# Kernel optimization log

Measured on AMD Instinct MI355X. Metric: run time of the kernel, lower is better.

Reference implementation:

```python
import jax, jax.numpy as jnp
import numpy as np

B, CIN, COUT, G, HEADS = 4, 256, 256, 8, 4
K, S, P = 7, 1, 3
H = W = 32
IN_W = CIN // G
OUT_W = COUT // G


def setup_inputs() -> dict:
    key = jax.random.key(0)
    ks = jax.random.split(key, 9)
    def n(k, shape, scale=1.0):
        return jax.random.normal(k, shape, dtype=jnp.float32) * scale
    # kaiming fan_out init for the 1x1 convs (fan_out = out channels)
    return {
        "x": n(ks[0], (B, CIN, H, W)),
        "wq": n(ks[1], (G, OUT_W * HEADS, IN_W), (2.0 / (OUT_W * HEADS)) ** 0.5),
        "bq": n(ks[2], (G, OUT_W * HEADS), 0.01),
        "wk": n(ks[3], (G, OUT_W, IN_W), (2.0 / OUT_W) ** 0.5),
        "bk": n(ks[4], (G, OUT_W), 0.01),
        "wv": n(ks[5], (G, OUT_W, IN_W), (2.0 / OUT_W) ** 0.5),
        "bv": n(ks[6], (G, OUT_W), 0.01),
        "rel_h": n(ks[7], (OUT_W // 2, 1, 1, G, K, 1)),
        "rel_w": n(ks[8], (OUT_W // 2, 1, 1, G, 1, K)),
    }


def _sparse_conv(x, w, b):
    # grouped 1x1 conv, groups stacked on last axis (matches torch.stack(dim=-1))
    # x: [B, G*I, h, w]; w: [G, O, I]; b: [G, O] -> [B, O, h, w, G]
    Bn, C, hh, ww = x.shape
    xr = x.reshape(Bn, G, C // G, hh, ww)
    out = jnp.einsum('bgihw,goi->bohwg', xr, w)
    return out + b.T[None, :, None, None, :]


def _unfold(x5, k, s):
    # x5: [B, C, Hp, Wp, G] -> [B, C, Ho, Wo, G, k, k]  (torch unfold(2).unfold(3))
    Bn, C, Hp, Wp, Gn = x5.shape
    Ho = (Hp - k) // s + 1
    Wo = (Wp - k) // s + 1
    patches = jnp.stack(
        [x5[:, :, i:i + (Ho - 1) * s + 1:s, j:j + (Wo - 1) * s + 1:s, :]
         for i in range(k) for j in range(k)], axis=-1)
    return patches.reshape(Bn, C, Ho, Wo, Gn, k, k)


def reference(x, wq, bq, wk, bk, wv, bv, rel_h, rel_w):
    xp = jnp.pad(x, ((0, 0), (0, 0), (P, P), (P, P)))
    q = _sparse_conv(x, wq, bq)    # [B, OUT_W*HEADS, H, W, G]
    k = _sparse_conv(xp, wk, bk)   # [B, OUT_W, Hp, Wp, G] (bias at padded locations, as in torch)
    v = _sparse_conv(xp, wv, bv)
    k = _unfold(k, K, S)           # [B, OUT_W, H, W, G, K, K]
    v = _unfold(v, K, S)
    kh, kw = jnp.split(k, 2, axis=1)
    k = jnp.concatenate([kh + rel_h, kw + rel_w], axis=1)
    kf = k.reshape(B, OUT_W, H, W, G * K * K)
    vf = v.reshape(B, OUT_W, H, W, G * K * K)
    q = q.reshape(B, HEADS, OUT_W, H, W, G)
    # scores: sum over channel c; softmax over flattened (group, kh, kw) window
    scores = jnp.einsum('bhcxyg,bcxym->bhxygm', q, kf)
    attn = jax.nn.softmax(scores, axis=-1)
    # weighted sum over window m and heads h (matches sum(dim=1) then sum(dim=-1))
    out = jnp.einsum('bhxygm,bcxym->bcxyg', attn, vf)   # [B, OUT_W, H, W, G]
    out = jnp.transpose(out, (0, 4, 2, 3, 1)).reshape(B, -1, H, W)  # transpose(1,-1)+reshape
    return out
```

## Files before the change

### kernel.cpp

```cpp
#include <hip/hip_runtime.h>
#include <math.h>

typedef _Float16 f16;
typedef _Float16 f16x4 __attribute__((ext_vector_type(4)));
typedef _Float16 f16x8 __attribute__((ext_vector_type(8)));
typedef __bf16 bf16x4 __attribute__((ext_vector_type(4)));
typedef __bf16 bf16x4a8 __attribute__((ext_vector_type(4), aligned(8)));
typedef short s16x4 __attribute__((ext_vector_type(4)));
typedef float f32x4 __attribute__((ext_vector_type(4)));

#define MFMA_F16(a, b, c)  __builtin_amdgcn_mfma_f32_16x16x32_f16(a, b, c, 0, 0, 0)
#define MFMA_BF16_K16(a, b, c) __builtin_amdgcn_mfma_f32_16x16x16bf16_1k(a, b, c, 0, 0, 0)

#define VSS 12160

static __device__ inline f16x8 cvt8(const float* p) {
    const float4* p4 = (const float4*)p;
    float4 u0 = p4[0], u1 = p4[1];
    f16x8 r;
    r[0] = (f16)u0.x; r[1] = (f16)u0.y; r[2] = (f16)u0.z; r[3] = (f16)u0.w;
    r[4] = (f16)u1.x; r[5] = (f16)u1.y; r[6] = (f16)u1.z; r[7] = (f16)u1.w;
    return r;
}

__global__ __launch_bounds__(256) void produce_kernel(
    const float* __restrict__ x,
    const float* __restrict__ wq, const float* __restrict__ bq,
    const float* __restrict__ wk, const float* __restrict__ bk,
    const float* __restrict__ wv, const float* __restrict__ bv,
    const float* __restrict__ rel_h, const float* __restrict__ rel_w,
    f16* __restrict__ Qb, f16* __restrict__ Kb,
    __bf16* __restrict__ V4, f16* __restrict__ relp) {
    int bid = blockIdx.x;
    int t = threadIdx.x;

    if (bid == 1216) {
        for (int idx = t; idx < 448 * 32; idx += 256) {
            int c = idx & 31, key = idx >> 5;
            int kw = key & 7, ghk = key >> 3;
            int gp = (ghk * 37) >> 8;
            int kh = ghk - gp * 7;
            float v = 0.f;
            if (kw < 7)
                v = (c < 16) ? rel_h[c * 56 + gp * 7 + kh]
                             : rel_w[(c - 16) * 56 + gp * 7 + kw];
            relp[idx] = (f16)v;
        }
        return;
    }

    int hp = bid % 38, g = (bid / 38) & 7, b = bid / 304;
    bool hin = (hp >= 3 && hp < 35);
    size_t kvbase = (size_t)(b * 8 + g);
    size_t rowp = (kvbase * 38 + hp) * 10;

    if (!hin) {
        for (int idx = t; idx < 38 * 32; idx += 256) {
            int wp = idx >> 5, c = idx & 31;
            Kb[((kvbase * 38 + hp) * 38 + wp) * 32 + c] = (f16)bk[g * 32 + c];
        }
        for (int idx = t; idx < 4 * 40 * 32; idx += 256) {
            int c = idx & 31, w = (idx >> 5) % 40, s = (idx >> 5) / 40;
            int wp = s + w;
            __bf16 val = (wp <= 37) ? (__bf16)bv[g * 32 + c] : (__bf16)0.f;
            V4[((size_t)s * VSS + rowp + (w >> 2)) * 128 + c * 4 + (w & 3)] = val;
        }
        return;
    }

    int h = hp - 3;
    __shared__ __align__(16) f16 xTl[32 * 40];
    __shared__ float vt[32 * 44];

    {
        int ic = t >> 3, w = (t & 7) * 4;
        float4 xv = *(const float4*)(x + (((size_t)b * 256 + g * 32 + ic) * 32 + h) * 32 + w);
        xTl[(w + 0) * 40 + ic] = (f16)xv.x;
        xTl[(w + 1) * 40 + ic] = (f16)xv.y;
        xTl[(w + 2) * 40 + ic] = (f16)xv.z;
        xTl[(w + 3) * 40 + ic] = (f16)xv.w;
    }
    for (int idx = t; idx < 384; idx += 256) {
        int c = idx & 31, wi = idx >> 5;
        float bb = bv[g * 32 + c];
        if (wi < 3) vt[c * 44 + wi] = bb;
        else if (wi < 6) vt[c * 44 + 32 + wi] = bb;
        else vt[c * 44 + 32 + wi] = 0.f;
    }
    __syncthreads();

    int l15 = t & 15, quad = (t >> 4) & 3, wave = t >> 6;

    f16x8 xf0 = *(const f16x8*)(xTl + l15 * 40 + quad * 8);
    f16x8 xf1 = *(const f16x8*)(xTl + (16 + l15) * 40 + quad * 8);

#pragma unroll
    for (int i = 0; i < 2; ++i) {
        int mq = wave * 2 + i;
        f16x8 wf = cvt8(wq + ((size_t)g * 128 + mq * 16 + l15) * 32 + quad * 8);
        float4 b4 = *(const float4*)(bq + g * 128 + mq * 16 + quad * 4);
#pragma unroll
        for (int Nt = 0; Nt < 2; ++Nt) {
            f32x4 d = {0.f, 0.f, 0.f, 0.f};
            d = MFMA_F16(wf, Nt ? xf1 : xf0, d);
            f16x4 q4;
            q4[0] = (f16)(d[0] + b4.x); q4[1] = (f16)(d[1] + b4.y);
            q4[2] = (f16)(d[2] + b4.z); q4[3] = (f16)(d[3] + b4.w);
            int w = Nt * 16 + l15;
            *(f16x4*)(Qb + (size_t)((b * 32 + h) * 32 + w) * 1024 + g * 128 + mq * 16 + quad * 4) = q4;
        }
    }

    if (wave < 2) {
        f16x8 wf = cvt8(wk + ((size_t)g * 32 + wave * 16 + l15) * 32 + quad * 8);
        float4 b4 = *(const float4*)(bk + g * 32 + wave * 16 + quad * 4);
#pragma unroll
        for (int Nt = 0; Nt < 2; ++Nt) {
            f32x4 d = {0.f, 0.f, 0.f, 0.f};
            d = MFMA_F16(wf, Nt ? xf1 : xf0, d);
            f16x4 k4;
            k4[0] = (f16)(d[0] + b4.x); k4[1] = (f16)(d[1] + b4.y);
            k4[2] = (f16)(d[2] + b4.z); k4[3] = (f16)(d[3] + b4.w);
            int wp = Nt * 16 + l15 + 3;
            *(f16x4*)(Kb + ((kvbase * 38 + hp) * 38 + wp) * 32 + wave * 16 + quad * 4) = k4;
        }
    } else {
        int Nt = wave - 2;
        f16x8 wf = cvt8(wv + ((size_t)g * 32 + Nt * 16 + l15) * 32 + quad * 8);
        float bias = bv[g * 32 + Nt * 16 + l15];
        int c = Nt * 16 + l15;
#pragma unroll
        for (int Mt = 0; Mt < 2; ++Mt) {
            f32x4 d = {0.f, 0.f, 0.f, 0.f};
            d = MFMA_F16(Mt ? xf1 : xf0, wf, d);
            int wp0 = Mt * 16 + quad * 4 + 3;
            vt[c * 44 + wp0 + 0] = d[0] + bias;
            vt[c * 44 + wp0 + 1] = d[1] + bias;
            vt[c * 44 + wp0 + 2] = d[2] + bias;
            vt[c * 44 + wp0 + 3] = d[3] + bias;
        }
    }

    for (int idx = t; idx < 192; idx += 256) {
        int wi = idx >> 5, c = idx & 31;
        int wp = (wi < 3) ? wi : (32 + wi);
        Kb[((kvbase * 38 + hp) * 38 + wp) * 32 + c] = (f16)bk[g * 32 + c];
    }
    __syncthreads();

    for (int idx = t; idx < 1280; idx += 256) {
        int c = idx & 31;
        int p = (idx >> 5) % 10;
        int s = (idx >> 5) / 10;
        const float* src = vt + c * 44 + s + p * 4;
        bf16x4a8 q;
        q[0] = (__bf16)src[0]; q[1] = (__bf16)src[1];
        q[2] = (__bf16)src[2]; q[3] = (__bf16)src[3];
        *(bf16x4a8*)(V4 + ((size_t)s * VSS + rowp + p) * 128 + c * 4) = q;
    }
}

__global__ __launch_bounds__(256, 4) void attn_kernel(
    const f16* __restrict__ Qb, const f16* __restrict__ Kb,
    const __bf16* __restrict__ V4, const f16* __restrict__ relp,
    float* __restrict__ out) {
    int bid = blockIdx.x;
    int t = threadIdx.x;
    int wvi = t >> 6;
    int pid = (bid & 7) * 512 + (bid >> 3);
    int y = pid & 31, x = (pid >> 5) & 31, b = pid >> 10;

    __shared__ __align__(16) float accS[3 * 64 * 20];

    int lane = t & 63;
    int l15 = lane & 15, quad = lane >> 4, kwl = lane & 7, p8 = (lane >> 3) & 1;
    bool oddq = (quad & 1);

    f16x8 qf[2];
    {
        const f16* qp = Qb + (size_t)pid * 1024;
        qf[0] = *(const f16x8*)(qp + l15 * 32 + quad * 8);
        qf[1] = *(const f16x8*)(qp + (16 + l15) * 32 + quad * 8);
    }

    float fsumT[2] = {0.f, 0.f};
    f32x4 acc[2][2];
#pragma unroll
    for (int ct = 0; ct < 2; ++ct)
#pragma unroll
        for (int m = 0; m < 2; ++m) acc[ct][m] = (f32x4){0.f, 0.f, 0.f, 0.f};

    int yk = y + kwl;
    if (yk > 37) yk = 37;
    size_t vshift = (size_t)(y & 3) * VSS;

    {
        int chunk = wvi;
        int gpr = chunk * 2 + p8;
        int gpv = chunk * 2 + (quad >> 1);
        const f16* kbp = Kb + ((((size_t)(b * 8 + gpr) * 38 + x) * 38 + yk) << 5) + quad * 8;
        const f16* rpp = relp + ((size_t)(gpr * 56 + kwl) << 5) + quad * 8;
        const __bf16* vp0 = V4 +
            ((vshift + ((size_t)(b * 8 + gpv) * 38 + x) * 10 + (y >> 2) + (quad & 1)) << 7) +
            l15 * 4;
        const __bf16* vp1 = vp0 + 64;
#pragma unroll
        for (int kh = 0; kh < 7; ++kh) {
            f16x8 kb = *(const f16x8*)kbp;  kbp += 38 * 32;
            f16x8 rp = *(const f16x8*)rpp;  rpp += 256;
            s16x4 vf0 = *(const s16x4*)vp0;  vp0 += 1280;
            s16x4 vf1 = *(const s16x4*)vp1;  vp1 += 1280;
            kb += rp;
#pragma unroll
            for (int Mt = 0; Mt < 2; ++Mt) {
                f32x4 d = {0.f, 0.f, 0.f, 0.f};
                d = MFMA_F16(kb, qf[Mt], d);
                float e0 = __expf(d[0]);
                float e1 = __expf(d[1]);
                float e2 = __expf(d[2]);
                float e3 = oddq ? 0.f : __expf(d[3]);
                fsumT[Mt] += (e0 + e1) + (e2 + e3);
                bf16x4 pb;
                pb[0] = (__bf16)e0; pb[1] = (__bf16)e1;
                pb[2] = (__bf16)e2; pb[3] = (__bf16)e3;
                s16x4 pbi = __builtin_bit_cast(s16x4, pb);
                acc[0][Mt] = MFMA_BF16_K16(vf0, pbi, acc[0][Mt]);
                acc[1][Mt] = MFMA_BF16_K16(vf1, pbi, acc[1][Mt]);
            }
        }
    }

#pragma unroll
    for (int m = 0; m < 2; ++m) {
        fsumT[m] += __shfl_xor(fsumT[m], 16);
        fsumT[m] += __shfl_xor(fsumT[m], 32);
    }

    if (wvi != 0) {
        float* sp = accS + ((wvi - 1) * 64 + lane) * 20;
        *(f32x4*)(sp + 0)  = acc[0][0];
        *(f32x4*)(sp + 4)  = acc[0][1];
        *(f32x4*)(sp + 8)  = acc[1][0];
        *(f32x4*)(sp + 12) = acc[1][1];
        sp[16] = fsumT[0];
        sp[17] = fsumT[1];
    }
    __syncthreads();
    if (wvi != 0) return;

#pragma unroll
    for (int wsrc = 0; wsrc < 3; ++wsrc) {
        const float* sp = accS + (wsrc * 64 + lane) * 20;
        acc[0][0] += *(const f32x4*)(sp + 0);
        acc[0][1] += *(const f32x4*)(sp + 4);
        acc[1][0] += *(const f32x4*)(sp + 8);
        acc[1][1] += *(const f32x4*)(sp + 12);
        fsumT[0] += sp[16];
        fsumT[1] += sp[17];
    }
    float inv[2] = {1.0f / fsumT[0], 1.0f / fsumT[1]};

#pragma unroll
    for (int Mt = 0; Mt < 2; ++Mt)
#pragma unroll
        for (int ct = 0; ct < 2; ++ct) {
            float v[4];
#pragma unroll
            for (int r = 0; r < 4; ++r) {
                v[r] = acc[ct][Mt][r] * inv[Mt];
                v[r] += __shfl_xor(v[r], 1);
                v[r] += __shfl_xor(v[r], 2);
            }
            if ((l15 & 3) == 0) {
                int g = Mt * 4 + (l15 >> 2);
                float4 o4 = {v[0], v[1], v[2], v[3]};
                *(float4*)(out + ((((size_t)(b * 8 + g) * 32 + x) * 32 + y) << 5) +
                           ct * 16 + quad * 4) = o4;
            }
        }
}

extern "C" void kernel_launch(void* const* d_in, const int* in_sizes, int n_in,
                              void* d_out, int out_size, void* d_ws, size_t ws_size,
                              hipStream_t stream) {
    const float* x     = (const float*)d_in[0];
    const float* wq    = (const float*)d_in[1];
    const float* bq    = (const float*)d_in[2];
    const float* wk    = (const float*)d_in[3];
    const float* bk    = (const float*)d_in[4];
    const float* wv    = (const float*)d_in[5];
    const float* bv    = (const float*)d_in[6];
    const float* rel_h = (const float*)d_in[7];
    const float* rel_w = (const float*)d_in[8];
    float* out = (float*)d_out;

    unsigned char* ws = (unsigned char*)d_ws;
    f16*    Qb   = (f16*)ws;
    f16*    Kb   = (f16*)(ws + 8388608);
    __bf16* V4   = (__bf16*)(ws + 8388608 + 2957312);
    f16*    relp = (f16*)(ws + 8388608 + 2957312 + 12451840);

    hipLaunchKernelGGL(produce_kernel, dim3(1217), dim3(256), 0, stream,
                       x, wq, bq, wk, bk, wv, bv, rel_h, rel_w, Qb, Kb, V4, relp);
    hipLaunchKernelGGL(attn_kernel, dim3(4096), dim3(256), 0, stream,
                       Qb, Kb, V4, relp, out);
}
```

Baseline: 120.4 us.

## Tile attention over 8 output columns with shared K/V windows in LDS

The attention kernel now handles 8 adjacent y positions per 512-thread block, with one wave per position instead of four waves per position. The overlapping K and V windows are staged once into LDS and reused across those positions. V is stored in a compact single-copy layout rather than four shifted copies, and the unaligned bf16 pairs are recovered with funnel-shift selects. The cross-wave LDS reduction is removed. In exchange, LDS use is large and occupancy falls to one block per CU.

Measured after the change: 121.6 us. About the same (+1.0%).

```diff
diff --git a/kernel.cpp b/kernel.cpp
--- a/kernel.cpp
+++ b/kernel.cpp
@@ -8,11 +8,10 @@
 typedef __bf16 bf16x4a8 __attribute__((ext_vector_type(4), aligned(8)));
 typedef short s16x4 __attribute__((ext_vector_type(4)));
 typedef float f32x4 __attribute__((ext_vector_type(4)));
+typedef unsigned int u32;
 
 #define MFMA_F16(a, b, c)  __builtin_amdgcn_mfma_f32_16x16x32_f16(a, b, c, 0, 0, 0)
 #define MFMA_BF16_K16(a, b, c) __builtin_amdgcn_mfma_f32_16x16x16bf16_1k(a, b, c, 0, 0, 0)
-
-#define VSS 12160
 
 static __device__ inline f16x8 cvt8(const float* p) {
     const float4* p4 = (const float4*)p;
@@ -23,6 +22,16 @@
     return r;
 }
 
+static __device__ inline u32 alignsel(u32 hi, u32 lo, u32 sh) {
+    return sh ? (u32)(((((unsigned long long)hi) << 32) | lo) >> sh) : lo;
+}
+
+static __device__ inline u32 pack2bf(float a, float b) {
+    __bf16 x0 = (__bf16)a, x1 = (__bf16)b;
+    return (u32)__builtin_bit_cast(unsigned short, x0) |
+           ((u32)__builtin_bit_cast(unsigned short, x1) << 16);
+}
+
 __global__ __launch_bounds__(256) void produce_kernel(
     const float* __restrict__ x,
     const float* __restrict__ wq, const float* __restrict__ bq,
@@ -30,20 +39,22 @@
     const float* __restrict__ wv, const float* __restrict__ bv,
     const float* __restrict__ rel_h, const float* __restrict__ rel_w,
     f16* __restrict__ Qb, f16* __restrict__ Kb,
-    __bf16* __restrict__ V4, f16* __restrict__ relp) {
+    __bf16* __restrict__ Vb, f16* __restrict__ relp) {
     int bid = blockIdx.x;
     int t = threadIdx.x;
 
     if (bid == 1216) {
-        for (int idx = t; idx < 448 * 32; idx += 256) {
-            int c = idx & 31, key = idx >> 5;
-            int kw = key & 7, ghk = key >> 3;
-            int gp = (ghk * 37) >> 8;
-            int kh = ghk - gp * 7;
-            float v = 0.f;
-            if (kw < 7)
-                v = (c < 16) ? rel_h[c * 56 + gp * 7 + kh]
-                             : rel_w[(c - 16) * 56 + gp * 7 + kw];
+        for (int idx = t; idx < 2944; idx += 256) {
+            float v;
+            if (idx < 896) {
+                int c = idx & 15, gk = idx >> 4;
+                v = rel_h[c * 56 + gk];
+            } else {
+                int i2 = idx - 896;
+                int c = i2 & 31, gw = i2 >> 5;
+                int g = gw >> 3, kw = gw & 7;
+                v = (c >= 16 && kw < 7) ? rel_w[(c - 16) * 56 + g * 7 + kw] : 0.f;
+            }
             relp[idx] = (f16)v;
         }
         return;
@@ -52,18 +63,19 @@
     int hp = bid % 38, g = (bid / 38) & 7, b = bid / 304;
     bool hin = (hp >= 3 && hp < 35);
     size_t kvbase = (size_t)(b * 8 + g);
-    size_t rowp = (kvbase * 38 + hp) * 10;
+    u32* Vb32 = (u32*)Vb;
 
     if (!hin) {
         for (int idx = t; idx < 38 * 32; idx += 256) {
             int wp = idx >> 5, c = idx & 31;
             Kb[((kvbase * 38 + hp) * 38 + wp) * 32 + c] = (f16)bk[g * 32 + c];
         }
-        for (int idx = t; idx < 4 * 40 * 32; idx += 256) {
-            int c = idx & 31, w = (idx >> 5) % 40, s = (idx >> 5) / 40;
-            int wp = s + w;
-            __bf16 val = (wp <= 37) ? (__bf16)bv[g * 32 + c] : (__bf16)0.f;
-            V4[((size_t)s * VSS + rowp + (w >> 2)) * 128 + c * 4 + (w & 3)] = val;
+        for (int idx = t; idx < 704; idx += 256) {
+            int c = idx / 22, dw = idx - c * 22;
+            float bb = bv[g * 32 + c];
+            float v0 = (dw * 2 <= 37) ? bb : 0.f;
+            float v1 = (dw * 2 + 1 <= 37) ? bb : 0.f;
+            Vb32[((kvbase * 38 + hp) * 32 + c) * 22 + dw] = pack2bf(v0, v1);
         }
         return;
     }
@@ -148,33 +160,34 @@
     }
     __syncthreads();
 
-    for (int idx = t; idx < 1280; idx += 256) {
-        int c = idx & 31;
-        int p = (idx >> 5) % 10;
-        int s = (idx >> 5) / 10;
-        const float* src = vt + c * 44 + s + p * 4;
-        bf16x4a8 q;
-        q[0] = (__bf16)src[0]; q[1] = (__bf16)src[1];
-        q[2] = (__bf16)src[2]; q[3] = (__bf16)src[3];
-        *(bf16x4a8*)(V4 + ((size_t)s * VSS + rowp + p) * 128 + c * 4) = q;
-    }
-}
-
-__global__ __launch_bounds__(256, 4) void attn_kernel(
+    for (int idx = t; idx < 704; idx += 256) {
+        int c = idx / 22, dw = idx - c * 22;
+        Vb32[((kvbase * 38 + hp) * 32 + c) * 22 + dw] =
+            pack2bf(vt[c * 44 + dw * 2], vt[c * 44 + dw * 2 + 1]);
+    }
+}
+
+__global__ __launch_bounds__(512, 1) void attn_kernel(
     const f16* __restrict__ Qb, const f16* __restrict__ Kb,
-    const __bf16* __restrict__ V4, const f16* __restrict__ relp,
+    const __bf16* __restrict__ Vb, const f16* __restrict__ relp,
     float* __restrict__ out) {
+    __shared__ __align__(16) f16 Klds[33600];
+    __shared__ __align__(16) __bf16 Vlds[35840];
+    __shared__ __align__(16) f16 Trw_l[2048];
+
     int bid = blockIdx.x;
     int t = threadIdx.x;
+    int G = (bid & 7) * 64 + (bid >> 3);
+    int yq = G & 3, x = (G >> 2) & 31, b = G >> 7;
+    int y0 = yq * 8;
+    int b8 = b * 8;
+
     int wvi = t >> 6;
-    int pid = (bid & 7) * 512 + (bid >> 3);
-    int y = pid & 31, x = (pid >> 5) & 31, b = pid >> 10;
-
-    __shared__ __align__(16) float accS[3 * 64 * 20];
-
     int lane = t & 63;
     int l15 = lane & 15, quad = lane >> 4, kwl = lane & 7, p8 = (lane >> 3) & 1;
     bool oddq = (quad & 1);
+    int y = y0 + wvi;
+    int pid = (b * 32 + x) * 32 + y;
 
     f16x8 qf[2];
     {
@@ -183,6 +196,28 @@
         qf[1] = *(const f16x8*)(qp + (16 + l15) * 32 + quad * 8);
     }
 
+    for (int i = t; i < 3360; i += 512) {
+        int row = i >> 2, q = i & 3;
+        int g = row / 105, r2 = row - g * 105;
+        int kh = r2 / 15, wpl = r2 - kh * 15;
+        int wp = y0 + wpl; if (wp > 37) wp = 37;
+        f16x8 kv = *(const f16x8*)(Kb + (((size_t)(b8 + g) * 38 + x + kh) * 38 + wp) * 32 + q * 8);
+        if (q < 2) kv += *(const f16x8*)(relp + (g * 7 + kh) * 16 + q * 8);
+        *(f16x8*)(Klds + row * 40 + q * 8) = kv;
+    }
+    for (int i = t; i < 8960; i += 512) {
+        int row = i / 5, j = i - row * 5;
+        int g = row / 224, r2 = row - g * 224;
+        int kh = r2 >> 5, c = r2 & 31;
+        uint2 v = *(const uint2*)(Vb + (((size_t)(b8 + g) * 38 + x + kh) * 32 + c) * 44 + y0 + j * 4);
+        *(uint2*)(Vlds + row * 20 + j * 4) = v;
+    }
+    {
+        int i = t;
+        *(uint2*)(Trw_l + i * 4) = *(const uint2*)(relp + 896 + i * 4);
+    }
+    __syncthreads();
+
     float fsumT[2] = {0.f, 0.f};
     f32x4 acc[2][2];
 #pragma unroll
@@ -190,27 +225,35 @@
 #pragma unroll
         for (int m = 0; m < 2; ++m) acc[ct][m] = (f32x4){0.f, 0.f, 0.f, 0.f};
 
-    int yk = y + kwl;
-    if (yk > 37) yk = 37;
-    size_t vshift = (size_t)(y & 3) * VSS;
-
-    {
-        int chunk = wvi;
+    int wpl37 = 37 - y0;
+    int wplk = wvi + kwl; if (wplk > wpl37) wplk = wpl37;
+    u32 shsel = (wvi & 1) ? 16u : 0u;
+    bool hi4 = (wvi & 2) != 0;
+    int eA = ((quad & 1) + (wvi >> 2)) * 4;
+
+#pragma unroll
+    for (int chunk = 0; chunk < 4; ++chunk) {
         int gpr = chunk * 2 + p8;
         int gpv = chunk * 2 + (quad >> 1);
-        const f16* kbp = Kb + ((((size_t)(b * 8 + gpr) * 38 + x) * 38 + yk) << 5) + quad * 8;
-        const f16* rpp = relp + ((size_t)(gpr * 56 + kwl) << 5) + quad * 8;
-        const __bf16* vp0 = V4 +
-            ((vshift + ((size_t)(b * 8 + gpv) * 38 + x) * 10 + (y >> 2) + (quad & 1)) << 7) +
-            l15 * 4;
-        const __bf16* vp1 = vp0 + 64;
+        f16x8 rp = *(const f16x8*)(Trw_l + (gpr * 8 + kwl) * 32 + quad * 8);
+        const f16* kp = Klds + (gpr * 105 + wplk) * 40 + quad * 8;
+        const __bf16* vb0 = Vlds + (size_t)gpv * 4480 + l15 * 20 + eA;
+        const __bf16* vb1 = vb0 + 320;
 #pragma unroll
         for (int kh = 0; kh < 7; ++kh) {
-            f16x8 kb = *(const f16x8*)kbp;  kbp += 38 * 32;
-            f16x8 rp = *(const f16x8*)rpp;  rpp += 256;
-            s16x4 vf0 = *(const s16x4*)vp0;  vp0 += 1280;
-            s16x4 vf1 = *(const s16x4*)vp1;  vp1 += 1280;
+            f16x8 kb = *(const f16x8*)kp;  kp += 600;
             kb += rp;
+            uint2 A0 = *(const uint2*)vb0;
+            uint2 B0 = *(const uint2*)(vb0 + 4);
+            uint2 A1 = *(const uint2*)vb1;
+            uint2 B1 = *(const uint2*)(vb1 + 4);
+            vb0 += 640; vb1 += 640;
+            u32 a0 = hi4 ? A0.y : A0.x, a1 = hi4 ? B0.x : A0.y, a2 = hi4 ? B0.y : B0.x;
+            s16x4 vf0 = __builtin_bit_cast(s16x4,
+                make_uint2(alignsel(a1, a0, shsel), alignsel(a2, a1, shsel)));
+            u32 c0 = hi4 ? A1.y : A1.x, c1 = hi4 ? B1.x : A1.y, c2 = hi4 ? B1.y : B1.x;
+            s16x4 vf1 = __builtin_bit_cast(s16x4,
+                make_uint2(alignsel(c1, c0, shsel), alignsel(c2, c1, shsel)));
 #pragma unroll
             for (int Mt = 0; Mt < 2; ++Mt) {
                 f32x4 d = {0.f, 0.f, 0.f, 0.f};
@@ -235,29 +278,6 @@
         fsumT[m] += __shfl_xor(fsumT[m], 16);
         fsumT[m] += __shfl_xor(fsumT[m], 32);
     }
-
-    if (wvi != 0) {
-        float* sp = accS + ((wvi - 1) * 64 + lane) * 20;
-        *(f32x4*)(sp + 0)  = acc[0][0];
-        *(f32x4*)(sp + 4)  = acc[0][1];
-        *(f32x4*)(sp + 8)  = acc[1][0];
-        *(f32x4*)(sp + 12) = acc[1][1];
-        sp[16] = fsumT[0];
-        sp[17] = fsumT[1];
-    }
-    __syncthreads();
-    if (wvi != 0) return;
-
-#pragma unroll
-    for (int wsrc = 0; wsrc < 3; ++wsrc) {
-        const float* sp = accS + (wsrc * 64 + lane) * 20;
-        acc[0][0] += *(const f32x4*)(sp + 0);
-        acc[0][1] += *(const f32x4*)(sp + 4);
-        acc[1][0] += *(const f32x4*)(sp + 8);
-        acc[1][1] += *(const f32x4*)(sp + 12);
-        fsumT[0] += sp[16];
-        fsumT[1] += sp[17];
-    }
     float inv[2] = {1.0f / fsumT[0], 1.0f / fsumT[1]};
 
 #pragma unroll
@@ -274,7 +294,7 @@
             if ((l15 & 3) == 0) {
                 int g = Mt * 4 + (l15 >> 2);
                 float4 o4 = {v[0], v[1], v[2], v[3]};
-                *(float4*)(out + ((((size_t)(b * 8 + g) * 32 + x) * 32 + y) << 5) +
+                *(float4*)(out + ((((size_t)(b8 + g) * 32 + x) * 32 + y) << 5) +
                            ct * 16 + quad * 4) = o4;
             }
         }
@@ -297,11 +317,11 @@
     unsigned char* ws = (unsigned char*)d_ws;
     f16*    Qb   = (f16*)ws;
     f16*    Kb   = (f16*)(ws + 8388608);
-    __bf16* V4   = (__bf16*)(ws + 8388608 + 2957312);
-    f16*    relp = (f16*)(ws + 8388608 + 2957312 + 12451840);
+    __bf16* Vb   = (__bf16*)(ws + 8388608 + 2957312);
+    f16*    relp = (f16*)(ws + 8388608 + 2957312 + 3424256);
 
     hipLaunchKernelGGL(produce_kernel, dim3(1217), dim3(256), 0, stream,
-                       x, wq, bq, wk, bk, wv, bv, rel_h, rel_w, Qb, Kb, V4, relp);
-    hipLaunchKernelGGL(attn_kernel, dim3(4096), dim3(256), 0, stream,
-                       Qb, Kb, V4, relp, out);
-}
+                       x, wq, bq, wk, bk, wv, bv, rel_h, rel_w, Qb, Kb, Vb, relp);
+    hipLaunchKernelGGL(attn_kernel, dim3(512), dim3(512), 0, stream,
+                       Qb, Kb, Vb, relp, out);
+}
```
